# Performance work log

Measured on AMD Instinct MI355X. Metric: run time of the kernel, lower is better.

## Reference

```python
import jax, jax.numpy as jnp
import numpy as np

B, N, NT, ET = 8, 38, 9, 4
R, E = 416, 378  # repeat_num, edge steps (E = R - N)
H = D = 128      # nhid, nout
L = 12           # num_flow_layer
GCN_LAYERS = 3
SHIFT = 2.0      # sigmoid_shift


def setup_inputs() -> dict:
    key = jax.random.key(0)
    ks = jax.random.split(key, 16)
    inp = {}
    inp['x'] = jax.random.normal(ks[0], (B, N, NT), jnp.float32)
    inp['adj'] = jax.random.normal(ks[1], (B, ET, N, N), jnp.float32)
    inp['x_deq'] = jax.random.normal(ks[2], (B, N, NT), jnp.float32)
    inp['adj_deq'] = jax.random.normal(ks[3], (B, E, ET), jnp.float32)
    inp['mask_node'] = jax.random.randint(ks[4], (R, N), 0, 2).astype(bool)
    inp['mask_edge'] = jax.random.randint(ks[5], (R, N, N), 0, 2).astype(bool)
    inp['index_select_edge'] = jax.random.randint(ks[6], (E, 2), 0, N)
    inp['emb_w'] = jax.random.normal(ks[7], (NT, H), jnp.float32) * 0.1
    inp['gc_w'] = jax.random.normal(ks[8], (GCN_LAYERS, ET - 1, H, H), jnp.float32) * 0.05
    inp['gc_b'] = jnp.zeros((GCN_LAYERS, H), jnp.float32)
    inp['nw1'] = jax.random.normal(ks[9], (L, D, H), jnp.float32) * 0.05
    inp['nb1'] = jnp.zeros((L, H), jnp.float32)
    inp['nw2'] = jax.random.normal(ks[10], (L, H, 2 * NT), jnp.float32) * 0.05
    inp['nb2'] = jnp.zeros((L, 2 * NT), jnp.float32)
    inp['ew1'] = jax.random.normal(ks[11], (L, 3 * D, H), jnp.float32) * 0.05
    inp['eb1'] = jnp.zeros((L, H), jnp.float32)
    inp['ew2'] = jax.random.normal(ks[12], (L, H, 2 * ET), jnp.float32) * 0.05
    inp['eb2'] = jnp.zeros((L, 2 * ET), jnp.float32)
    return inp


def _get_embs(x, adj, mask_node, mask_edge, index_select_edge, emb_w, gc_w, gc_b):
    # mask + repeat: (B,R,N,NT) and (B,R,3,N,N), flattened to B*R graphs
    adj3 = adj[:, :ET - 1]
    xm = jnp.where(mask_node[None, :, :, None], x[:, None, :, :], 0.0)
    xm = xm.reshape(B * R, N, NT)
    am = jnp.where(mask_edge[None, :, None, :, :], adj3[:, None, :, :, :], 0.0)
    am = am.reshape(B * R, ET - 1, N, N)
    # relational GCN: emb then per-relation conv, summed over relations
    h = xm @ emb_w  # (BR, N, H)
    for l in range(GCN_LAYERS):
        sup = jnp.einsum('bni,eio->beno', h, gc_w[l])      # (BR, 3, N, H)
        out = jnp.einsum('benm,bemo->bno', am, sup) + gc_b[l]
        h = jax.nn.relu(out) if l < GCN_LAYERS - 1 else out
    node_emb = h.reshape(B, R, N, D)
    graph_emb = node_emb.sum(axis=2)                        # (B, R, D)
    g_node = graph_emb[:, :N].reshape(B * N, D)
    g_edge = graph_emb[:, N:]                               # (B, E, D)
    ne = node_emb[:, N:]                                    # (B, E, N, D)
    idx = jnp.broadcast_to(index_select_edge[None, :, :, None], (B, E, 2, D))
    pairs = jnp.take_along_axis(ne, idx, axis=2)            # (B, E, 2, D)
    g_ne = jnp.concatenate([pairs, g_edge[:, :, None, :]], axis=2)
    return g_node, g_ne.reshape(B * E, 3 * D)


def _st(inp, w1, b1, w2, b2, out_dim):
    st = jnp.tanh(inp @ w1 + b1) @ w2 + b2
    s = jax.nn.sigmoid(st[:, :out_dim] + SHIFT)
    t = st[:, out_dim:]
    return s, t


def reference(x, adj, x_deq, adj_deq, mask_node, mask_edge, index_select_edge,
              emb_w, gc_w, gc_b, nw1, nb1, nw2, nb2, ew1, eb1, ew2, eb2):
    g_node, g_edge = _get_embs(x, adj, mask_node, mask_edge, index_select_edge,
                               emb_w, gc_w, gc_b)
    xd = x_deq.reshape(-1, NT)
    ad = adj_deq.reshape(-1, ET)
    xlj = jnp.zeros_like(xd)
    alj = jnp.zeros_like(ad)
    for i in range(L):
        ns, nt = _st(g_node, nw1[i], nb1[i], nw2[i], nb2[i], NT)
        xd = xd * ns + nt
        xlj = xlj + jnp.log(jnp.abs(ns) + 1e-20)
        es, et = _st(g_edge, ew1[i], eb1[i], ew2[i], eb2[i], ET)
        ad = ad * es + et
        alj = alj + jnp.log(jnp.abs(es) + 1e-20)
    return (xd.reshape(B, -1), ad.reshape(B, -1),
            xlj.reshape(B, -1).sum(-1), alj.reshape(B, -1).sum(-1))
```

## Files before the change

kernel.cpp:

```cpp
#include <hip/hip_runtime.h>
#include <stdint.h>
#include <math.h>

#define Bc   8
#define Nn   38
#define NTc  9
#define ETc  4
#define Rr   416
#define Ee   378
#define Hh   128
#define Ll   12
#define GL   3

typedef __attribute__((ext_vector_type(8))) short s16x8;
typedef __attribute__((ext_vector_type(4))) short s16x4;
typedef __attribute__((ext_vector_type(4))) float f32x4;

static const size_t WS_MN    = 0;
static const size_t WS_ME    = 15872;
static const size_t WS_H0    = 616576;
static const size_t WS_ST    = 772224;
static const size_t WS_GWT   = 1165440;
static const size_t WS_NWT   = 1460352;
static const size_t WS_EWT   = 1853568;
static const size_t WS_GNB   = 3033216;
static const size_t WS_GEDGE = 3111040;
static const size_t WS_SN    = 5433472;
static const size_t WS_TN    = 5564800;
static const size_t WS_SE    = 5696128;
static const size_t WS_TE    = 6276736;
static const size_t WS_PART  = 6857344;

__device__ __forceinline__ unsigned short f2bf(float f) {
  unsigned u = __float_as_uint(f);
  u += 0x7FFFu + ((u >> 16) & 1u);
  return (unsigned short)(u >> 16);
}
__device__ __forceinline__ float bf2f(unsigned short h) {
  return __uint_as_float(((unsigned)h) << 16);
}

__device__ __forceinline__ uint8_t mval(const void* src, int i, int mode) {
  if (mode == 0) return ((const int*)src)[i] != 0;
  if (mode == 1) return ((const float*)src)[i] != 0.0f;
  return ((const uint8_t*)src)[i] != 0;
}

__global__ void prep_masks(const void* __restrict__ mn_src, const void* __restrict__ me_src,
                           uint8_t* __restrict__ mn_dst, uint8_t* __restrict__ me_dst)
{
  __shared__ int s01, sf;
  if (threadIdx.x == 0) { s01 = 1; sf = 1; }
  __syncthreads();
  const uint32_t* p = (const uint32_t*)me_src;
  bool a01 = true, af = true;
  for (int i = threadIdx.x; i < 256; i += blockDim.x) {
    uint32_t v = p[i];
    if (v > 1u) a01 = false;
    if (v != 0u && v != 0x3f800000u) af = false;
  }
  if (!a01) atomicAnd(&s01, 0);
  if (!af)  atomicAnd(&sf, 0);
  __syncthreads();
  const int mode = s01 ? 0 : (sf ? 1 : 2);

  const int n_node = Rr * Nn;
  const int n_edge = Rr * Nn * Nn;
  const int tot = n_node + n_edge;
  for (int i = blockIdx.x * blockDim.x + threadIdx.x; i < tot; i += gridDim.x * blockDim.x) {
    if (i < n_node) mn_dst[i] = mval(mn_src, i, mode);
    else            me_dst[i - n_node] = mval(me_src, i - n_node, mode);
  }
}

__global__ void prep_weights(const float* __restrict__ gw, const float* __restrict__ nw1,
                             const float* __restrict__ ew1,
                             unsigned short* __restrict__ gwt, unsigned short* __restrict__ nwt,
                             unsigned short* __restrict__ ewt)
{
  const int NG = 9 * 128 * 128;
  const int NNw = 12 * 128 * 128;
  const int NEw = 12 * 128 * 384;
  int idx = blockIdx.x * blockDim.x + threadIdx.x;
  if (idx < NG) {
    int k = idx & 127, col = (idx >> 7) & 127, le = idx >> 14;
    gwt[idx] = f2bf(gw[((size_t)le * 128 + k) * 128 + col]);
  } else if (idx < NG + NNw) {
    int j = idx - NG;
    int k = j & 127, col = (j >> 7) & 127, i = j >> 14;
    nwt[j] = f2bf(nw1[((size_t)i * 128 + k) * 128 + col]);
  } else if (idx < NG + NNw + NEw) {
    int j = idx - NG - NNw;
    int k = j % 384; int rem = j / 384;
    int col = rem & 127, i = rem >> 7;
    ewt[j] = f2bf(ew1[((size_t)i * 384 + k) * 128 + col]);
  }
}

__global__ void h0_kernel(const float* __restrict__ x, const float* __restrict__ emb_w,
                          float* __restrict__ h0)
{
  int idx = blockIdx.x * blockDim.x + threadIdx.x;
  if (idx >= Bc * Nn * Hh) return;
  int bn = idx >> 7, o = idx & 127;
  float acc = 0.0f;
  #pragma unroll
  for (int i = 0; i < NTc; ++i) acc += x[bn * NTc + i] * emb_w[i * Hh + o];
  h0[idx] = acc;
}

__global__ void s_kernel(const float* __restrict__ h0, const float* __restrict__ gw,
                         unsigned short* __restrict__ St)
{
  int idx = blockIdx.x * blockDim.x + threadIdx.x;
  if (idx >= Bc * GL * Hh * 64) return;
  int m = idx & 63;
  int col = (idx >> 6) & 127;
  int t = idx >> 13;
  int e = t % GL, b = t / GL;
  float acc = 0.0f;
  if (m < Nn)
    for (int k = 0; k < Hh; ++k)
      acc += h0[(b * Nn + m) * Hh + k] * gw[((size_t)e * Hh + k) * Hh + col];
  St[idx] = (m < Nn) ? f2bf(acc) : (unsigned short)0;
}

__global__ __launch_bounds__(256, 3)
void gcn_mfma_kernel(const float* __restrict__ adj, const uint8_t* __restrict__ mn,
                     const uint8_t* __restrict__ me, const unsigned short* __restrict__ St,
                     const unsigned short* __restrict__ gwt, const float* __restrict__ gb,
                     const int* __restrict__ isel,
                     unsigned short* __restrict__ gnb, unsigned short* __restrict__ gedge)
{
  __shared__ char smem[47744];
  unsigned short* h_lds  = (unsigned short*)smem;
  unsigned short* supT   = (unsigned short*)(smem + 12288);
  unsigned short* am_lds = (unsigned short*)(smem + 28672);
  float*          ge     = (float*)(smem + 47104);
  unsigned char*  mnu    = (unsigned char*)(smem + 47616);

  const int tid = threadIdx.x;
  const int b = blockIdx.x / Rr;
  const int r = blockIdx.x - b * Rr;
  const int lane = tid & 63;
  const int wv = tid >> 6;
  const int lo = lane & 15;
  const int q  = lane >> 4;
  const int swz = (lo & 7) << 3;
  const int ct0 = 2 * wv;

  for (int idx = tid; idx < GL * 48 * 64; idx += 256) {
    int e = idx / (48 * 64);
    int rem = idx - e * (48 * 64);
    int n = rem >> 6, m = rem & 63;
    float v = 0.0f;
    if (n < Nn && m < Nn && me[r * (Nn * Nn) + n * Nn + m])
      v = adj[((b * ETc + e) * Nn + n) * Nn + m];
    am_lds[e * 3072 + n * 64 + (m ^ ((n & 7) << 3))] = f2bf(v);
  }
  if (tid < 64) mnu[tid] = (tid < Nn) ? mn[r * Nn + tid] : 0;

  {
    int zcol = tid >> 1, zhalf = tid & 1;
    int zsw = (zcol & 7) << 3;
    *(s16x8*)&supT[zcol * 64 + ((48 + 8 * zhalf) ^ zsw)] = (s16x8){0,0,0,0,0,0,0,0};
  }
  __syncthreads();

  uint32_t mkm[2][4];
  #pragma unroll
  for (int ks = 0; ks < 2; ++ks)
    #pragma unroll
    for (int d = 0; d < 4; ++d) {
      int k0 = 32 * ks + 8 * q + 2 * d;
      mkm[ks][d] = (mnu[k0] ? 0x0000FFFFu : 0u) | (mnu[k0 + 1] ? 0xFFFF0000u : 0u);
    }

  float bias[GL][2];
  #pragma unroll
  for (int l = 0; l < GL; ++l)
    #pragma unroll
    for (int ci = 0; ci < 2; ++ci)
      bias[l][ci] = gb[l * Hh + 16 * (ct0 + ci) + lo];

  f32x4 outacc[3][2];

  #pragma unroll
  for (int ci = 0; ci < 2; ++ci) {
    f32x4 bv = {bias[0][ci], bias[0][ci], bias[0][ci], bias[0][ci]};
    outacc[0][ci] = bv; outacc[1][ci] = bv; outacc[2][ci] = bv;
  }
  #pragma unroll
  for (int e = 0; e < GL; ++e) {
    const unsigned short* Sb = St + (size_t)(b * GL + e) * 128 * 64;
    #pragma unroll
    for (int ks = 0; ks < 2; ++ks) {
      union { s16x8 v; uint32_t u[4]; } B0, B1;
      B0.v = *(const s16x8*)(Sb + (16 * ct0 + lo) * 64 + 32 * ks + 8 * q);
      B1.v = *(const s16x8*)(Sb + (16 * ct0 + 16 + lo) * 64 + 32 * ks + 8 * q);
      #pragma unroll
      for (int d = 0; d < 4; ++d) { B0.u[d] &= mkm[ks][d]; B1.u[d] &= mkm[ks][d]; }
      #pragma unroll
      for (int rt = 0; rt < 3; ++rt) {
        s16x8 a = *(const s16x8*)&am_lds[e * 3072 + (lo + 16 * rt) * 64 + ((8 * q + 32 * ks) ^ swz)];
        outacc[rt][0] = __builtin_amdgcn_mfma_f32_16x16x32_bf16(a, B0.v, outacc[rt][0], 0, 0, 0);
        outacc[rt][1] = __builtin_amdgcn_mfma_f32_16x16x32_bf16(a, B1.v, outacc[rt][1], 0, 0, 0);
      }
    }
  }
  #pragma unroll
  for (int rt = 0; rt < 3; ++rt)
    #pragma unroll
    for (int ci = 0; ci < 2; ++ci) {
      int col = 16 * (ct0 + ci) + lo;
      #pragma unroll
      for (int j = 0; j < 4; ++j) {
        int row = 16 * rt + 4 * q + j;
        h_lds[row * 128 + (col ^ ((row & 7) << 3))] = f2bf(fmaxf(outacc[rt][ci][j], 0.0f));
      }
    }
  __syncthreads();

  #pragma unroll
  for (int l = 1; l < GL; ++l) {
    #pragma unroll
    for (int ci = 0; ci < 2; ++ci) {
      f32x4 bv = {bias[l][ci], bias[l][ci], bias[l][ci], bias[l][ci]};
      outacc[0][ci] = bv; outacc[1][ci] = bv; outacc[2][ci] = bv;
    }

    for (int e = 0; e < GL; ++e) {
      f32x4 sa[3][2];
      #pragma unroll
      for (int rt = 0; rt < 3; ++rt)
        #pragma unroll
        for (int ci = 0; ci < 2; ++ci)
          sa[rt][ci] = (f32x4){0.f, 0.f, 0.f, 0.f};

      const unsigned short* wb = gwt + (size_t)(l * GL + e) * (Hh * Hh);
      #pragma unroll
      for (int ks = 0; ks < 4; ++ks) {
        int k0 = 8 * q + 32 * ks;
        s16x8 b0 = *(const s16x8*)(wb + (16 * ct0 + lo) * 128 + k0);
        s16x8 b1 = *(const s16x8*)(wb + (16 * ct0 + 16 + lo) * 128 + k0);
        #pragma unroll
        for (int rt = 0; rt < 3; ++rt) {
          s16x8 a = *(const s16x8*)&h_lds[(lo + 16 * rt) * 128 + (k0 ^ swz)];
          sa[rt][0] = __builtin_amdgcn_mfma_f32_16x16x32_bf16(a, b0, sa[rt][0], 0, 0, 0);
          sa[rt][1] = __builtin_amdgcn_mfma_f32_16x16x32_bf16(a, b1, sa[rt][1], 0, 0, 0);
        }
      }

      #pragma unroll
      for (int rt = 0; rt < 3; ++rt)
        #pragma unroll
        for (int ci = 0; ci < 2; ++ci) {
          int col = 16 * (ct0 + ci) + lo;
          s16x4 pk;
          #pragma unroll
          for (int j = 0; j < 4; ++j) pk[j] = (short)f2bf(sa[rt][ci][j]);
          int k0 = 16 * rt + 4 * q;
          *(s16x4*)&supT[col * 64 + (k0 ^ swz)] = pk;
        }

      #pragma unroll
      for (int ks = 0; ks < 2; ++ks) {
        int k0 = 8 * q + 32 * ks;
        s16x8 b0 = *(const s16x8*)&supT[(16 * ct0 + lo) * 64 + (k0 ^ swz)];
        s16x8 b1 = *(const s16x8*)&supT[(16 * ct0 + 16 + lo) * 64 + (k0 ^ swz)];
        #pragma unroll
        for (int rt = 0; rt < 3; ++rt) {
          s16x8 a = *(const s16x8*)&am_lds[e * 3072 + (lo + 16 * rt) * 64 + (k0 ^ swz)];
          outacc[rt][0] = __builtin_amdgcn_mfma_f32_16x16x32_bf16(a, b0, outacc[rt][0], 0, 0, 0);
          outacc[rt][1] = __builtin_amdgcn_mfma_f32_16x16x32_bf16(a, b1, outacc[rt][1], 0, 0, 0);
        }
      }
    }

    __syncthreads();
    #pragma unroll
    for (int rt = 0; rt < 3; ++rt)
      #pragma unroll
      for (int ci = 0; ci < 2; ++ci) {
        int col = 16 * (ct0 + ci) + lo;
        #pragma unroll
        for (int j = 0; j < 4; ++j) {
          int row = 16 * rt + 4 * q + j;
          float v = outacc[rt][ci][j];
          if (l < GL - 1) v = fmaxf(v, 0.0f);
          h_lds[row * 128 + (col ^ ((row & 7) << 3))] = f2bf(v);
        }
      }
    __syncthreads();
  }

  if (tid < 128) {
    float s = 0.0f;
    for (int n = 0; n < Nn; ++n)
      s += bf2f(h_lds[n * 128 + (tid ^ ((n & 7) << 3))]);
    ge[tid] = s;
  }
  __syncthreads();

  if (r < Nn) {
    if (tid < 128) gnb[(size_t)(b * Nn + r) * Hh + tid] = f2bf(ge[tid]);
  } else {
    int ei = r - Nn;
    int i0 = isel[2 * ei], i1 = isel[2 * ei + 1];
    unsigned short* dst = gedge + (size_t)(b * Ee + ei) * 384;
    if (tid < 128) {
      dst[tid]        = h_lds[i0 * 128 + (tid ^ ((i0 & 7) << 3))];
      dst[128 + tid]  = h_lds[i1 * 128 + (tid ^ ((i1 & 7) << 3))];
      dst[256 + tid]  = f2bf(ge[tid]);
    }
  }
}

template<int IN_W, int OUT_D, int ROWS>
__global__ __launch_bounds__(256)
void st_mfma_kernel(const unsigned short* __restrict__ A,
                    const unsigned short* __restrict__ wt,
                    const float* __restrict__ b1,
                    const float* __restrict__ w2,
                    const float* __restrict__ b2,
                    float* __restrict__ s_out, float* __restrict__ t_out)
{
  constexpr int MT = (ROWS + 31) / 32;
  constexpr int OD2 = 2 * OUT_D;
  __shared__ unsigned short hid[32 * 136];
  const int tid = threadIdx.x;
  const int i = blockIdx.x / MT;
  const int mt = blockIdx.x - i * MT;
  const int row0 = mt * 32;
  const int lane = tid & 63, wv = tid >> 6;
  const int lo = lane & 15, q = lane >> 4;

  f32x4 acc[2][2];
  #pragma unroll
  for (int rt = 0; rt < 2; ++rt)
    #pragma unroll
    for (int ci = 0; ci < 2; ++ci)
      acc[rt][ci] = (f32x4){0.f, 0.f, 0.f, 0.f};

  int ra = row0 + lo;       if (ra >= ROWS) ra = 0;
  int rb = row0 + 16 + lo;  if (rb >= ROWS) rb = 0;
  const unsigned short* Ap0 = A + (size_t)ra * IN_W;
  const unsigned short* Ap1 = A + (size_t)rb * IN_W;
  const unsigned short* Bp0 = wt + ((size_t)i * 128 + 32 * wv + lo) * IN_W;
  const unsigned short* Bp1 = wt + ((size_t)i * 128 + 32 * wv + 16 + lo) * IN_W;

  #pragma unroll
  for (int ks = 0; ks < IN_W / 32; ++ks) {
    int k0 = 8 * q + 32 * ks;
    s16x8 a0 = *(const s16x8*)(Ap0 + k0);
    s16x8 a1 = *(const s16x8*)(Ap1 + k0);
    s16x8 b0 = *(const s16x8*)(Bp0 + k0);
    s16x8 b1 = *(const s16x8*)(Bp1 + k0);
    acc[0][0] = __builtin_amdgcn_mfma_f32_16x16x32_bf16(a0, b0, acc[0][0], 0, 0, 0);
    acc[0][1] = __builtin_amdgcn_mfma_f32_16x16x32_bf16(a0, b1, acc[0][1], 0, 0, 0);
    acc[1][0] = __builtin_amdgcn_mfma_f32_16x16x32_bf16(a1, b0, acc[1][0], 0, 0, 0);
    acc[1][1] = __builtin_amdgcn_mfma_f32_16x16x32_bf16(a1, b1, acc[1][1], 0, 0, 0);
  }

  #pragma unroll
  for (int rt = 0; rt < 2; ++rt)
    #pragma unroll
    for (int ci = 0; ci < 2; ++ci) {
      int col = 32 * wv + 16 * ci + lo;
      float bb = b1[i * 128 + col];
      #pragma unroll
      for (int j = 0; j < 4; ++j) {
        int row = 16 * rt + 4 * q + j;
        hid[row * 136 + col] = f2bf(tanhf(acc[rt][ci][j] + bb));
      }
    }
  __syncthreads();

  for (int idx = tid; idx < 32 * OD2; idx += 256) {
    int lr = idx / OD2, c = idx - lr * OD2;
    int gr = row0 + lr;
    if (gr < ROWS) {
      float a = b2[i * OD2 + c];
      for (int k = 0; k < 128; ++k)
        a += bf2f(hid[lr * 136 + k]) * w2[((size_t)i * 128 + k) * OD2 + c];
      if (c < OUT_D) s_out[((size_t)i * ROWS + gr) * OUT_D + c] = 1.0f / (1.0f + expf(-(a + 2.0f)));
      else           t_out[((size_t)i * ROWS + gr) * OUT_D + (c - OUT_D)] = a;
    }
  }
}

__global__ __launch_bounds__(256)
void combine_part(const float* __restrict__ x_deq, const float* __restrict__ adj_deq,
                  const float* __restrict__ sn, const float* __restrict__ tn,
                  const float* __restrict__ se, const float* __restrict__ te,
                  float* __restrict__ out, float* __restrict__ partials)
{
  const int blk = blockIdx.x, tid = threadIdx.x;
  const int b = blk >> 3, ch = blk & 7;
  float ljx = 0.0f, lja = 0.0f;

  for (int j = ch * 256 + tid; j < Nn * NTc; j += 2048) {
    int n = j / NTc, c = j - n * NTc;
    int row = b * Nn + n;
    float v = x_deq[b * (Nn * NTc) + j];
    #pragma unroll
    for (int i = 0; i < Ll; ++i) {
      float s = sn[((size_t)i * (Bc * Nn) + row) * NTc + c];
      float t = tn[((size_t)i * (Bc * Nn) + row) * NTc + c];
      v = v * s + t;
      ljx += logf(fabsf(s) + 1e-20f);
    }
    out[b * (Nn * NTc) + j] = v;
  }

  for (int j = ch * 256 + tid; j < Ee * ETc; j += 2048) {
    int e = j / ETc, c = j - e * ETc;
    int row = b * Ee + e;
    float v = adj_deq[b * (Ee * ETc) + j];
    #pragma unroll
    for (int i = 0; i < Ll; ++i) {
      float s = se[((size_t)i * (Bc * Ee) + row) * ETc + c];
      float t = te[((size_t)i * (Bc * Ee) + row) * ETc + c];
      v = v * s + t;
      lja += logf(fabsf(s) + 1e-20f);
    }
    out[Bc * Nn * NTc + b * (Ee * ETc) + j] = v;
  }

  __shared__ float red[256];
  red[tid] = ljx; __syncthreads();
  for (int st = 128; st > 0; st >>= 1) { if (tid < st) red[tid] += red[tid + st]; __syncthreads(); }
  if (tid == 0) partials[blk] = red[0];
  __syncthreads();
  red[tid] = lja; __syncthreads();
  for (int st = 128; st > 0; st >>= 1) { if (tid < st) red[tid] += red[tid + st]; __syncthreads(); }
  if (tid == 0) partials[64 + blk] = red[0];
}

__global__ void combine_lj(const float* __restrict__ partials, float* __restrict__ out)
{
  int tid = threadIdx.x;
  if (tid < Bc) {
    float sx = 0.0f, sa = 0.0f;
    #pragma unroll
    for (int ch = 0; ch < 8; ++ch) {
      sx += partials[tid * 8 + ch];
      sa += partials[64 + tid * 8 + ch];
    }
    out[Bc * Nn * NTc + Bc * Ee * ETc + tid] = sx;
    out[Bc * Nn * NTc + Bc * Ee * ETc + Bc + tid] = sa;
  }
}

extern "C" void kernel_launch(void* const* d_in, const int* in_sizes, int n_in,
                              void* d_out, int out_size, void* d_ws, size_t ws_size,
                              hipStream_t stream)
{
  const float* x       = (const float*)d_in[0];
  const float* adj     = (const float*)d_in[1];
  const float* x_deq   = (const float*)d_in[2];
  const float* adj_deq = (const float*)d_in[3];
  const void*  mn_src  = d_in[4];
  const void*  me_src  = d_in[5];
  const int*   isel    = (const int*)d_in[6];
  const float* emb_w   = (const float*)d_in[7];
  const float* gw      = (const float*)d_in[8];
  const float* gb      = (const float*)d_in[9];
  const float* nw1     = (const float*)d_in[10];
  const float* nb1     = (const float*)d_in[11];
  const float* nw2     = (const float*)d_in[12];
  const float* nb2     = (const float*)d_in[13];
  const float* ew1     = (const float*)d_in[14];
  const float* eb1     = (const float*)d_in[15];
  const float* ew2     = (const float*)d_in[16];
  const float* eb2     = (const float*)d_in[17];

  char* ws = (char*)d_ws;
  uint8_t* mn            = (uint8_t*)(ws + WS_MN);
  uint8_t* me            = (uint8_t*)(ws + WS_ME);
  float* h0              = (float*)(ws + WS_H0);
  unsigned short* St     = (unsigned short*)(ws + WS_ST);
  unsigned short* gwt    = (unsigned short*)(ws + WS_GWT);
  unsigned short* nwt    = (unsigned short*)(ws + WS_NWT);
  unsigned short* ewt    = (unsigned short*)(ws + WS_EWT);
  unsigned short* gnb    = (unsigned short*)(ws + WS_GNB);
  unsigned short* gedge  = (unsigned short*)(ws + WS_GEDGE);
  float* sn              = (float*)(ws + WS_SN);
  float* tn              = (float*)(ws + WS_TN);
  float* se              = (float*)(ws + WS_SE);
  float* te              = (float*)(ws + WS_TE);
  float* partials        = (float*)(ws + WS_PART);

  const int NW_TOT = 9 * 128 * 128 + 12 * 128 * 128 + 12 * 128 * 384;

  prep_masks<<<256, 256, 0, stream>>>(mn_src, me_src, mn, me);
  prep_weights<<<(NW_TOT + 255) / 256, 256, 0, stream>>>(gw, nw1, ew1, gwt, nwt, ewt);
  h0_kernel<<<(Bc * Nn * Hh + 255) / 256, 256, 0, stream>>>(x, emb_w, h0);
  s_kernel<<<(Bc * GL * Hh * 64 + 255) / 256, 256, 0, stream>>>(h0, gw, St);
  gcn_mfma_kernel<<<Bc * Rr, 256, 0, stream>>>(adj, mn, me, St, gwt, gb, isel, gnb, gedge);
  st_mfma_kernel<128, NTc, Bc * Nn><<<Ll * ((Bc * Nn + 31) / 32), 256, 0, stream>>>(
      gnb, nwt, nb1, nw2, nb2, sn, tn);
  st_mfma_kernel<384, ETc, Bc * Ee><<<Ll * ((Bc * Ee + 31) / 32), 256, 0, stream>>>(
      gedge, ewt, eb1, ew2, eb2, se, te);
  combine_part<<<Bc * 8, 256, 0, stream>>>(x_deq, adj_deq, sn, tn, se, te, (float*)d_out, partials);
  combine_lj<<<1, 64, 0, stream>>>(partials, (float*)d_out);
}
```

Before: 330.5 us.

## Pre-pad adjacency and edge masks, vectorize GCN staging, transpose MFMA operands

The edge mask is pre-expanded into a padded 48x64 byte layout per repeat, and the masked adjacency slices are pre-converted to padded bf16 once in the weight-prep kernel. The GCN kernel can then stage its adjacency tile with 8-wide vector loads plus a select, instead of scalar fp32 and byte gathers in every block. The MFMA operand roles are swapped so each lane's accumulator holds four consecutive feature columns. That allows packed 4-element LDS stores of h and vector bias loads. The workspace layout is reshuffled so the later s/t buffers reuse the mask region, which relies on the kernels running in stream order.

Result: faster. 291.7 us (-11.7%).

```diff
diff --git a/kernel.cpp b/kernel.cpp
--- a/kernel.cpp
+++ b/kernel.cpp
@@ -17,19 +17,20 @@
 typedef __attribute__((ext_vector_type(4))) float f32x4;
 
 static const size_t WS_MN    = 0;
-static const size_t WS_ME    = 15872;
-static const size_t WS_H0    = 616576;
-static const size_t WS_ST    = 772224;
-static const size_t WS_GWT   = 1165440;
-static const size_t WS_NWT   = 1460352;
-static const size_t WS_EWT   = 1853568;
-static const size_t WS_GNB   = 3033216;
-static const size_t WS_GEDGE = 3111040;
-static const size_t WS_SN    = 5433472;
-static const size_t WS_TN    = 5564800;
-static const size_t WS_SE    = 5696128;
-static const size_t WS_TE    = 6276736;
-static const size_t WS_PART  = 6857344;
+static const size_t WS_MEP   = 15872;
+static const size_t WS_SN    = 15872;
+static const size_t WS_TN    = 147200;
+static const size_t WS_SE    = 278528;
+static const size_t WS_TE    = 859136;
+static const size_t WS_PART  = 1439744;
+static const size_t WS_H0    = 1293824;
+static const size_t WS_ST    = 1449472;
+static const size_t WS_GWT   = 1842688;
+static const size_t WS_NWT   = 2137600;
+static const size_t WS_EWT   = 2530816;
+static const size_t WS_ADJP  = 3710464;
+static const size_t WS_GNB   = 3857920;
+static const size_t WS_GEDGE = 3935744;
 
 __device__ __forceinline__ unsigned short f2bf(float f) {
   unsigned u = __float_as_uint(f);
@@ -47,7 +48,7 @@
 }
 
 __global__ void prep_masks(const void* __restrict__ mn_src, const void* __restrict__ me_src,
-                           uint8_t* __restrict__ mn_dst, uint8_t* __restrict__ me_dst)
+                           uint8_t* __restrict__ mn_dst, uint8_t* __restrict__ mep)
 {
   __shared__ int s01, sf;
   if (threadIdx.x == 0) { s01 = 1; sf = 1; }
@@ -65,22 +66,31 @@
   const int mode = s01 ? 0 : (sf ? 1 : 2);
 
   const int n_node = Rr * Nn;
-  const int n_edge = Rr * Nn * Nn;
-  const int tot = n_node + n_edge;
-  for (int i = blockIdx.x * blockDim.x + threadIdx.x; i < tot; i += gridDim.x * blockDim.x) {
-    if (i < n_node) mn_dst[i] = mval(mn_src, i, mode);
-    else            me_dst[i - n_node] = mval(me_src, i - n_node, mode);
+  const int n_pad  = Rr * 48 * 64;
+  for (int i = blockIdx.x * blockDim.x + threadIdx.x; i < n_node + n_pad;
+       i += gridDim.x * blockDim.x) {
+    if (i < n_node) {
+      mn_dst[i] = mval(mn_src, i, mode);
+    } else {
+      int j = i - n_node;
+      int m = j & 63, n = (j >> 6) & 47 - 0, r = j >> 6;
+      n = (j >> 6) % 48; r = j / (48 * 64);
+      uint8_t v = 0;
+      if (n < Nn && m < Nn) v = mval(me_src, r * (Nn * Nn) + n * Nn + m, mode);
+      mep[j] = v;
+    }
   }
 }
 
 __global__ void prep_weights(const float* __restrict__ gw, const float* __restrict__ nw1,
-                             const float* __restrict__ ew1,
+                             const float* __restrict__ ew1, const float* __restrict__ adj,
                              unsigned short* __restrict__ gwt, unsigned short* __restrict__ nwt,
-                             unsigned short* __restrict__ ewt)
-{
-  const int NG = 9 * 128 * 128;
+                             unsigned short* __restrict__ ewt, unsigned short* __restrict__ adjp)
+{
+  const int NG  = 9 * 128 * 128;
   const int NNw = 12 * 128 * 128;
   const int NEw = 12 * 128 * 384;
+  const int NA  = Bc * GL * 48 * 64;
   int idx = blockIdx.x * blockDim.x + threadIdx.x;
   if (idx < NG) {
     int k = idx & 127, col = (idx >> 7) & 127, le = idx >> 14;
@@ -94,6 +104,13 @@
     int k = j % 384; int rem = j / 384;
     int col = rem & 127, i = rem >> 7;
     ewt[j] = f2bf(ew1[((size_t)i * 384 + k) * 128 + col]);
+  } else if (idx < NG + NNw + NEw + NA) {
+    int j = idx - NG - NNw - NEw;
+    int m = j & 63, n = (j >> 6) % 48, be = j / (48 * 64);
+    int e = be % GL, b = be / GL;
+    unsigned short v = 0;
+    if (n < Nn && m < Nn) v = f2bf(adj[((b * ETc + e) * Nn + n) * Nn + m]);
+    adjp[j] = v;
   }
 }
 
@@ -126,8 +143,8 @@
 }
 
 __global__ __launch_bounds__(256, 3)
-void gcn_mfma_kernel(const float* __restrict__ adj, const uint8_t* __restrict__ mn,
-                     const uint8_t* __restrict__ me, const unsigned short* __restrict__ St,
+void gcn_mfma_kernel(const unsigned short* __restrict__ adjp, const uint8_t* __restrict__ mn,
+                     const uint8_t* __restrict__ mep, const unsigned short* __restrict__ St,
                      const unsigned short* __restrict__ gwt, const float* __restrict__ gb,
                      const int* __restrict__ isel,
                      unsigned short* __restrict__ gnb, unsigned short* __restrict__ gedge)
@@ -149,14 +166,17 @@
   const int swz = (lo & 7) << 3;
   const int ct0 = 2 * wv;
 
-  for (int idx = tid; idx < GL * 48 * 64; idx += 256) {
-    int e = idx / (48 * 64);
-    int rem = idx - e * (48 * 64);
-    int n = rem >> 6, m = rem & 63;
-    float v = 0.0f;
-    if (n < Nn && m < Nn && me[r * (Nn * Nn) + n * Nn + m])
-      v = adj[((b * ETc + e) * Nn + n) * Nn + m];
-    am_lds[e * 3072 + n * 64 + (m ^ ((n & 7) << 3))] = f2bf(v);
+  for (int idx = tid; idx < GL * 48 * 8; idx += 256) {
+    int e = idx / (48 * 8);
+    int rem = idx - e * 384;
+    int n = rem >> 3, m0 = (rem & 7) * 8;
+    uint64_t mb = *(const uint64_t*)&mep[(size_t)r * 3072 + n * 64 + m0];
+    s16x8 av = *(const s16x8*)&adjp[((size_t)(b * GL + e) * 48 + n) * 64 + m0];
+    s16x8 o;
+    #pragma unroll
+    for (int i = 0; i < 8; ++i)
+      o[i] = ((mb >> (8 * i)) & 0xffu) ? av[i] : (short)0;
+    *(s16x8*)&am_lds[e * 3072 + n * 64 + (m0 ^ ((n & 7) << 3))] = o;
   }
   if (tid < 64) mnu[tid] = (tid < Nn) ? mn[r * Nn + tid] : 0;
 
@@ -176,48 +196,42 @@
       mkm[ks][d] = (mnu[k0] ? 0x0000FFFFu : 0u) | (mnu[k0 + 1] ? 0xFFFF0000u : 0u);
     }
 
-  float bias[GL][2];
-  #pragma unroll
-  for (int l = 0; l < GL; ++l)
-    #pragma unroll
-    for (int ci = 0; ci < 2; ++ci)
-      bias[l][ci] = gb[l * Hh + 16 * (ct0 + ci) + lo];
-
-  f32x4 outacc[3][2];
+  f32x4 acc[3][2];
 
   #pragma unroll
   for (int ci = 0; ci < 2; ++ci) {
-    f32x4 bv = {bias[0][ci], bias[0][ci], bias[0][ci], bias[0][ci]};
-    outacc[0][ci] = bv; outacc[1][ci] = bv; outacc[2][ci] = bv;
+    f32x4 b4 = *(const f32x4*)&gb[16 * (ct0 + ci) + 4 * q];
+    acc[0][ci] = b4; acc[1][ci] = b4; acc[2][ci] = b4;
   }
   #pragma unroll
   for (int e = 0; e < GL; ++e) {
     const unsigned short* Sb = St + (size_t)(b * GL + e) * 128 * 64;
     #pragma unroll
     for (int ks = 0; ks < 2; ++ks) {
-      union { s16x8 v; uint32_t u[4]; } B0, B1;
-      B0.v = *(const s16x8*)(Sb + (16 * ct0 + lo) * 64 + 32 * ks + 8 * q);
-      B1.v = *(const s16x8*)(Sb + (16 * ct0 + 16 + lo) * 64 + 32 * ks + 8 * q);
-      #pragma unroll
-      for (int d = 0; d < 4; ++d) { B0.u[d] &= mkm[ks][d]; B1.u[d] &= mkm[ks][d]; }
-      #pragma unroll
-      for (int rt = 0; rt < 3; ++rt) {
-        s16x8 a = *(const s16x8*)&am_lds[e * 3072 + (lo + 16 * rt) * 64 + ((8 * q + 32 * ks) ^ swz)];
-        outacc[rt][0] = __builtin_amdgcn_mfma_f32_16x16x32_bf16(a, B0.v, outacc[rt][0], 0, 0, 0);
-        outacc[rt][1] = __builtin_amdgcn_mfma_f32_16x16x32_bf16(a, B1.v, outacc[rt][1], 0, 0, 0);
+      int m0 = 32 * ks + 8 * q;
+      union { s16x8 v; uint32_t u[4]; } A0, A1;
+      A0.v = *(const s16x8*)(Sb + (16 * ct0 + lo) * 64 + m0);
+      A1.v = *(const s16x8*)(Sb + (16 * (ct0 + 1) + lo) * 64 + m0);
+      #pragma unroll
+      for (int d = 0; d < 4; ++d) { A0.u[d] &= mkm[ks][d]; A1.u[d] &= mkm[ks][d]; }
+      #pragma unroll
+      for (int nt = 0; nt < 3; ++nt) {
+        s16x8 bf = *(const s16x8*)&am_lds[e * 3072 + (16 * nt + lo) * 64 + (m0 ^ swz)];
+        acc[nt][0] = __builtin_amdgcn_mfma_f32_16x16x32_bf16(A0.v, bf, acc[nt][0], 0, 0, 0);
+        acc[nt][1] = __builtin_amdgcn_mfma_f32_16x16x32_bf16(A1.v, bf, acc[nt][1], 0, 0, 0);
       }
     }
   }
   #pragma unroll
-  for (int rt = 0; rt < 3; ++rt)
+  for (int nt = 0; nt < 3; ++nt)
     #pragma unroll
     for (int ci = 0; ci < 2; ++ci) {
-      int col = 16 * (ct0 + ci) + lo;
-      #pragma unroll
-      for (int j = 0; j < 4; ++j) {
-        int row = 16 * rt + 4 * q + j;
-        h_lds[row * 128 + (col ^ ((row & 7) << 3))] = f2bf(fmaxf(outacc[rt][ci][j], 0.0f));
-      }
+      int n = 16 * nt + lo;
+      int c0 = 16 * (ct0 + ci) + 4 * q;
+      s16x4 pk;
+      #pragma unroll
+      for (int j = 0; j < 4; ++j) pk[j] = (short)f2bf(fmaxf(acc[nt][ci][j], 0.0f));
+      *(s16x4*)&h_lds[n * 128 + (c0 ^ ((n & 7) << 3))] = pk;
     }
   __syncthreads();
 
@@ -225,8 +239,8 @@
   for (int l = 1; l < GL; ++l) {
     #pragma unroll
     for (int ci = 0; ci < 2; ++ci) {
-      f32x4 bv = {bias[l][ci], bias[l][ci], bias[l][ci], bias[l][ci]};
-      outacc[0][ci] = bv; outacc[1][ci] = bv; outacc[2][ci] = bv;
+      f32x4 b4 = *(const f32x4*)&gb[l * Hh + 16 * (ct0 + ci) + 4 * q];
+      acc[0][ci] = b4; acc[1][ci] = b4; acc[2][ci] = b4;
     }
 
     for (int e = 0; e < GL; ++e) {
@@ -265,31 +279,33 @@
 
       #pragma unroll
       for (int ks = 0; ks < 2; ++ks) {
-        int k0 = 8 * q + 32 * ks;
-        s16x8 b0 = *(const s16x8*)&supT[(16 * ct0 + lo) * 64 + (k0 ^ swz)];
-        s16x8 b1 = *(const s16x8*)&supT[(16 * ct0 + 16 + lo) * 64 + (k0 ^ swz)];
+        int m0 = 32 * ks + 8 * q;
+        s16x8 A2a = *(const s16x8*)&supT[(16 * ct0 + lo) * 64 + (m0 ^ swz)];
+        s16x8 A2b = *(const s16x8*)&supT[(16 * (ct0 + 1) + lo) * 64 + (m0 ^ swz)];
         #pragma unroll
-        for (int rt = 0; rt < 3; ++rt) {
-          s16x8 a = *(const s16x8*)&am_lds[e * 3072 + (lo + 16 * rt) * 64 + (k0 ^ swz)];
-          outacc[rt][0] = __builtin_amdgcn_mfma_f32_16x16x32_bf16(a, b0, outacc[rt][0], 0, 0, 0);
-          outacc[rt][1] = __builtin_amdgcn_mfma_f32_16x16x32_bf16(a, b1, outacc[rt][1], 0, 0, 0);
+        for (int nt = 0; nt < 3; ++nt) {
+          s16x8 bf = *(const s16x8*)&am_lds[e * 3072 + (16 * nt + lo) * 64 + (m0 ^ swz)];
+          acc[nt][0] = __builtin_amdgcn_mfma_f32_16x16x32_bf16(A2a, bf, acc[nt][0], 0, 0, 0);
+          acc[nt][1] = __builtin_amdgcn_mfma_f32_16x16x32_bf16(A2b, bf, acc[nt][1], 0, 0, 0);
         }
       }
     }
 
     __syncthreads();
     #pragma unroll
-    for (int rt = 0; rt < 3; ++rt)
+    for (int nt = 0; nt < 3; ++nt)
       #pragma unroll
       for (int ci = 0; ci < 2; ++ci) {
-        int col = 16 * (ct0 + ci) + lo;
+        int n = 16 * nt + lo;
+        int c0 = 16 * (ct0 + ci) + 4 * q;
+        s16x4 pk;
         #pragma unroll
         for (int j = 0; j < 4; ++j) {
-          int row = 16 * rt + 4 * q + j;
-          float v = outacc[rt][ci][j];
+          float v = acc[nt][ci][j];
           if (l < GL - 1) v = fmaxf(v, 0.0f);
-          h_lds[row * 128 + (col ^ ((row & 7) << 3))] = f2bf(v);
+          pk[j] = (short)f2bf(v);
         }
+        *(s16x4*)&h_lds[n * 128 + (c0 ^ ((n & 7) << 3))] = pk;
       }
     __syncthreads();
   }
@@ -477,12 +493,13 @@
 
   char* ws = (char*)d_ws;
   uint8_t* mn            = (uint8_t*)(ws + WS_MN);
-  uint8_t* me            = (uint8_t*)(ws + WS_ME);
+  uint8_t* mep           = (uint8_t*)(ws + WS_MEP);
   float* h0              = (float*)(ws + WS_H0);
   unsigned short* St     = (unsigned short*)(ws + WS_ST);
   unsigned short* gwt    = (unsigned short*)(ws + WS_GWT);
   unsigned short* nwt    = (unsigned short*)(ws + WS_NWT);
   unsigned short* ewt    = (unsigned short*)(ws + WS_EWT);
+  unsigned short* adjp   = (unsigned short*)(ws + WS_ADJP);
   unsigned short* gnb    = (unsigned short*)(ws + WS_GNB);
   unsigned short* gedge  = (unsigned short*)(ws + WS_GEDGE);
   float* sn              = (float*)(ws + WS_SN);
@@ -491,13 +508,13 @@
   float* te              = (float*)(ws + WS_TE);
   float* partials        = (float*)(ws + WS_PART);
 
-  const int NW_TOT = 9 * 128 * 128 + 12 * 128 * 128 + 12 * 128 * 384;
-
-  prep_masks<<<256, 256, 0, stream>>>(mn_src, me_src, mn, me);
-  prep_weights<<<(NW_TOT + 255) / 256, 256, 0, stream>>>(gw, nw1, ew1, gwt, nwt, ewt);
+  const int NW_TOT = 9 * 128 * 128 + 12 * 128 * 128 + 12 * 128 * 384 + Bc * GL * 48 * 64;
+
+  prep_masks<<<256, 256, 0, stream>>>(mn_src, me_src, mn, mep);
+  prep_weights<<<(NW_TOT + 255) / 256, 256, 0, stream>>>(gw, nw1, ew1, adj, gwt, nwt, ewt, adjp);
   h0_kernel<<<(Bc * Nn * Hh + 255) / 256, 256, 0, stream>>>(x, emb_w, h0);
   s_kernel<<<(Bc * GL * Hh * 64 + 255) / 256, 256, 0, stream>>>(h0, gw, St);
-  gcn_mfma_kernel<<<Bc * Rr, 256, 0, stream>>>(adj, mn, me, St, gwt, gb, isel, gnb, gedge);
+  gcn_mfma_kernel<<<Bc * Rr, 256, 0, stream>>>(adjp, mn, mep, St, gwt, gb, isel, gnb, gedge);
   st_mfma_kernel<128, NTc, Bc * Nn><<<Ll * ((Bc * Nn + 31) / 32), 256, 0, stream>>>(
       gnb, nwt, nb1, nw2, nb2, sn, tn);
   st_mfma_kernel<384, ETc, Bc * Ee><<<Ll * ((Bc * Ee + 31) / 32), 256, 0, stream>>>(
```
